# Kernel optimization log

Measured on AMD Instinct MI355X. Metric: run time of the kernel, lower is better.

The kernel has to match this reference:

```python
import jax, jax.numpy as jnp
import numpy as np

LSH_BUCKETS = 32
LSH_BANDWIDTH = 2.0
N_HASHES = 4
K_MAX = 64


def setup_inputs() -> dict:
    key0 = jax.random.key(0)
    kq, kk, kw = jax.random.split(key0, 3)
    B, L, D = 4, 4096, 64
    query = jax.random.normal(kq, (B, L, D), dtype=jnp.float32)
    key = jax.random.normal(kk, (B, L, D), dtype=jnp.float32)
    # learned LSH projection: maps binary features (D) -> N_HASHES hash values
    W = jax.random.normal(kw, (D, N_HASHES), dtype=jnp.float32)
    return {"query": query, "key": key, "W": W, "head_idx": 0}


def _lsh_hash(x_bin, W):
    # standard E2LSH-style hash: floor(<x, w> / bandwidth) mod n_buckets
    proj = x_bin @ W  # (B, L, N_HASHES)
    return jnp.floor(proj / LSH_BANDWIDTH).astype(jnp.int32) % LSH_BUCKETS


def reference(query, key, W, head_idx):
    B, L, _ = query.shape
    # binary_quantize: (x > 0).float()
    q_bin = (query > 0).astype(query.dtype)
    k_bin = (key > 0).astype(key.dtype)
    qh = _lsh_hash(q_bin, W)  # (B, L, N_HASHES) ints in [0, LSH_BUCKETS)
    kh = _lsh_hash(k_bin, W)
    # pack the N_HASHES hash values into one integer code per token;
    # codes equal  <=>  all hash values equal (values are in [0, LSH_BUCKETS))
    radix = (LSH_BUCKETS ** jnp.arange(N_HASHES)).astype(jnp.int32)  # (N_HASHES,)
    q_code = jnp.sum(qh * radix, axis=-1)  # (B, L)
    k_code = jnp.sum(kh * radix, axis=-1)  # (B, L)
    # match[b, i, j] = all hashes of query i equal hashes of key j
    match = q_code[:, :, None] == k_code[:, None, :]  # (B, L, L) bool
    # collect first K_MAX matching j per (b, i), pad with -1 (matches the
    # sequential early-break loop since j is scanned in increasing order)
    j_idx = jnp.arange(L, dtype=jnp.int32)
    score = jnp.where(match, j_idx[None, None, :], L)  # non-matches pushed to end
    first = jnp.sort(score, axis=-1)[:, :, :K_MAX]      # (B, L, K_MAX)
    candidates = jnp.where(first < L, first, -1)        # int32 indices, -1 pad
    return candidates
```

## Files before the change

### kernel.cpp

```cpp
#include <hip/hip_runtime.h>

#define KMAX 64
#define BB 4
#define LL 4096
#define DD 64
#define TOK (BB * LL)
#define QPW 4

typedef unsigned long long u64;

__global__ __launch_bounds__(256) void codes_kernel(
        const float* __restrict__ q,
        const float* __restrict__ k,
        const float* __restrict__ W,
        int* __restrict__ codes ) {
    __shared__ float sW[DD * 4];
    int tid = threadIdx.x;
    sW[tid] = W[tid];
    __syncthreads();

    int u = blockIdx.x * 256 + tid;
    const float* src = (u < TOK) ? q : k;
    int t = u & (TOK - 1);

    const float4* xp = (const float4*)(src + (size_t)t * DD);
    float4 x[16];
    #pragma unroll
    for (int i = 0; i < 16; ++i) x[i] = xp[i];

    float p0 = 0.f, p1 = 0.f, p2 = 0.f, p3 = 0.f;
    const float4* wrow = (const float4*)sW;
    #pragma unroll
    for (int d = 0; d < DD; ++d) {
        float xv = ((const float*)x)[d];
        float b = (xv > 0.f) ? 1.0f : 0.0f;
        float4 w = wrow[d];
        p0 = fmaf(b, w.x, p0);
        p1 = fmaf(b, w.y, p1);
        p2 = fmaf(b, w.z, p2);
        p3 = fmaf(b, w.w, p3);
    }
    int h0 = ((int)floorf(p0 * 0.5f)) & 31;
    int h1 = ((int)floorf(p1 * 0.5f)) & 31;
    int h2 = ((int)floorf(p2 * 0.5f)) & 31;
    int h3 = ((int)floorf(p3 * 0.5f)) & 31;
    codes[u] = h0 | (h1 << 5) | (h2 << 10) | (h3 << 15);
}

__global__ __launch_bounds__(256) void find_kernel(
        const int* __restrict__ qcodes,
        const int* __restrict__ kcodes,
        int* __restrict__ out) {
    int gtid = blockIdx.x * 256 + threadIdx.x;
    int wave = gtid >> 6;
    int lane = gtid & 63;
    int qbase = wave * QPW;
    int b = qbase >> 12;
    const int4* kc4 = (const int4*)(kcodes + b * LL);
    const int* qp = qcodes + qbase;
    int* outb = out + (size_t)qbase * KMAX;
    u64 lowmask = (1ull << lane) - 1ull;

    int4 kv[16];
    #pragma unroll
    for (int g = 0; g < 16; ++g) kv[g] = kc4[g * 64 + lane];

    int qc[QPW], cnt[QPW];
    #pragma unroll
    for (int i = 0; i < QPW; ++i) { qc[i] = qp[i]; cnt[i] = 0; }

    #pragma unroll
    for (int g = 0; g < 16; ++g) {
        bool a0 = (kv[g].x == qc[0]) | (kv[g].y == qc[0]) | (kv[g].z == qc[0]) | (kv[g].w == qc[0]);
        bool a1 = (kv[g].x == qc[1]) | (kv[g].y == qc[1]) | (kv[g].z == qc[1]) | (kv[g].w == qc[1]);
        bool a2 = (kv[g].x == qc[2]) | (kv[g].y == qc[2]) | (kv[g].z == qc[2]) | (kv[g].w == qc[2]);
        bool a3 = (kv[g].x == qc[3]) | (kv[g].y == qc[3]) | (kv[g].z == qc[3]) | (kv[g].w == qc[3]);
        if (__ballot(a0 | a1 | a2 | a3) == 0) continue;
        int j0 = g * 256 + lane * 4;
        #pragma unroll
        for (int i = 0; i < QPW; ++i) {
            if (cnt[i] >= KMAX) continue;
            bool m0 = (kv[g].x == qc[i]), m1 = (kv[g].y == qc[i]);
            bool m2 = (kv[g].z == qc[i]), m3 = (kv[g].w == qc[i]);
            if (__ballot(m0 | m1 | m2 | m3) == 0) continue;
            u64 b0 = __ballot(m0), b1 = __ballot(m1);
            u64 b2 = __ballot(m2), b3 = __ballot(m3);
            int before = __popcll(b0 & lowmask) + __popcll(b1 & lowmask)
                       + __popcll(b2 & lowmask) + __popcll(b3 & lowmask);
            int pos = cnt[i] + before;
            int* op = outb + i * KMAX;
            if (m0) { if (pos < KMAX) op[pos] = j0;     ++pos; }
            if (m1) { if (pos < KMAX) op[pos] = j0 + 1; ++pos; }
            if (m2) { if (pos < KMAX) op[pos] = j0 + 2; ++pos; }
            if (m3) { if (pos < KMAX) op[pos] = j0 + 3; ++pos; }
            cnt[i] += __popcll(b0) + __popcll(b1) + __popcll(b2) + __popcll(b3);
        }
    }
    #pragma unroll
    for (int i = 0; i < QPW; ++i) {
        int p = cnt[i] + lane;
        if (p < KMAX) outb[i * KMAX + p] = -1;
    }
}

extern "C" void kernel_launch(void* const* d_in, const int* in_sizes, int n_in,
                              void* d_out, int out_size, void* d_ws, size_t ws_size,
                              hipStream_t stream) {
    const float* q = (const float*)d_in[0];
    const float* k = (const float*)d_in[1];
    const float* W = (const float*)d_in[2];
    int* out = (int*)d_out;
    int* codes = (int*)d_ws;
    int* qcodes = codes;
    int* kcodes = codes + TOK;

    codes_kernel<<<(2 * TOK) / 256, 256, 0, stream>>>(q, k, W, codes);

    const int total_threads = (TOK / QPW) * 64;
    find_kernel<<<total_threads / 256, 256, 0, stream>>>(qcodes, kcodes, out);
}
```

Measured before the change: 20.90 us.

## Fuse query hash computation into the find kernel; hash only keys separately

Result: slower. 23.17 us (+10.9%).

```diff
diff --git a/kernel.cpp b/kernel.cpp
--- a/kernel.cpp
+++ b/kernel.cpp
@@ -9,21 +9,18 @@
 
 typedef unsigned long long u64;
 
-__global__ __launch_bounds__(256) void codes_kernel(
-        const float* __restrict__ q,
+__global__ __launch_bounds__(64) void kcodes_kernel(
         const float* __restrict__ k,
         const float* __restrict__ W,
-        int* __restrict__ codes ) {
+        int* __restrict__ kcodes ) {
     __shared__ float sW[DD * 4];
-    int tid = threadIdx.x;
-    sW[tid] = W[tid];
+    int lane = threadIdx.x;
+    #pragma unroll
+    for (int i = 0; i < 4; ++i) sW[i * 64 + lane] = W[i * 64 + lane];
     __syncthreads();
 
-    int u = blockIdx.x * 256 + tid;
-    const float* src = (u < TOK) ? q : k;
-    int t = u & (TOK - 1);
-
-    const float4* xp = (const float4*)(src + (size_t)t * DD);
+    int t = blockIdx.x * 64 + lane;
+    const float4* xp = (const float4*)(k + (size_t)t * DD);
     float4 x[16];
     #pragma unroll
     for (int i = 0; i < 16; ++i) x[i] = xp[i];
@@ -44,62 +41,96 @@
     int h1 = ((int)floorf(p1 * 0.5f)) & 31;
     int h2 = ((int)floorf(p2 * 0.5f)) & 31;
     int h3 = ((int)floorf(p3 * 0.5f)) & 31;
-    codes[u] = h0 | (h1 << 5) | (h2 << 10) | (h3 << 15);
+    kcodes[t] = h0 | (h1 << 5) | (h2 << 10) | (h3 << 15);
 }
 
 __global__ __launch_bounds__(256) void find_kernel(
-        const int* __restrict__ qcodes,
+        const float* __restrict__ q,
+        const float* __restrict__ W,
         const int* __restrict__ kcodes,
         int* __restrict__ out) {
-    int gtid = blockIdx.x * 256 + threadIdx.x;
+    __shared__ float sW[DD * 4];
+    int tid = threadIdx.x;
+    sW[tid] = W[tid];
+    __syncthreads();
+
+    int gtid = blockIdx.x * 256 + tid;
     int wave = gtid >> 6;
     int lane = gtid & 63;
     int qbase = wave * QPW;
     int b = qbase >> 12;
-    const int4* kc4 = (const int4*)(kcodes + b * LL);
-    const int* qp = qcodes + qbase;
-    int* outb = out + (size_t)qbase * KMAX;
-    u64 lowmask = (1ull << lane) - 1ull;
 
-    int4 kv[16];
-    #pragma unroll
-    for (int g = 0; g < 16; ++g) kv[g] = kc4[g * 64 + lane];
+    {
+        int myq = qbase + (lane >> 4);
+        const float4* xp = (const float4*)(q + (size_t)myq * DD);
+        float4 x[16];
+        #pragma unroll
+        for (int i = 0; i < 16; ++i) x[i] = xp[i];
+        float p0 = 0.f, p1 = 0.f, p2 = 0.f, p3 = 0.f;
+        const float4* wrow = (const float4*)sW;
+        #pragma unroll
+        for (int d = 0; d < DD; ++d) {
+            float xv = ((const float*)x)[d];
+            float bq = (xv > 0.f) ? 1.0f : 0.0f;
+            float4 w = wrow[d];
+            p0 = fmaf(bq, w.x, p0);
+            p1 = fmaf(bq, w.y, p1);
+            p2 = fmaf(bq, w.z, p2);
+            p3 = fmaf(bq, w.w, p3);
+        }
+        int h0 = ((int)floorf(p0 * 0.5f)) & 31;
+        int h1 = ((int)floorf(p1 * 0.5f)) & 31;
+        int h2 = ((int)floorf(p2 * 0.5f)) & 31;
+        int h3 = ((int)floorf(p3 * 0.5f)) & 31;
+        int mycode = h0 | (h1 << 5) | (h2 << 10) | (h3 << 15);
+        int c0 = __shfl(mycode, 0, 64);
+        int c1 = __shfl(mycode, 16, 64);
+        int c2 = __shfl(mycode, 32, 64);
+        int c3 = __shfl(mycode, 48, 64);
+        int qc_[QPW] = {c0, c1, c2, c3};
+        int cnt_[QPW] = {0, 0, 0, 0};
 
-    int qc[QPW], cnt[QPW];
-    #pragma unroll
-    for (int i = 0; i < QPW; ++i) { qc[i] = qp[i]; cnt[i] = 0; }
+        const int4* kc4 = (const int4*)(kcodes + b * LL);
+        int* outb = out + (size_t)qbase * KMAX;
+        u64 lowmask = (1ull << lane) - 1ull;
 
-    #pragma unroll
-    for (int g = 0; g < 16; ++g) {
-        bool a0 = (kv[g].x == qc[0]) | (kv[g].y == qc[0]) | (kv[g].z == qc[0]) | (kv[g].w == qc[0]);
-        bool a1 = (kv[g].x == qc[1]) | (kv[g].y == qc[1]) | (kv[g].z == qc[1]) | (kv[g].w == qc[1]);
-        bool a2 = (kv[g].x == qc[2]) | (kv[g].y == qc[2]) | (kv[g].z == qc[2]) | (kv[g].w == qc[2]);
-        bool a3 = (kv[g].x == qc[3]) | (kv[g].y == qc[3]) | (kv[g].z == qc[3]) | (kv[g].w == qc[3]);
-        if (__ballot(a0 | a1 | a2 | a3) == 0) continue;
-        int j0 = g * 256 + lane * 4;
+        int4 kv[16];
+        #pragma unroll
+        for (int g = 0; g < 16; ++g) kv[g] = kc4[g * 64 + lane];
+
+        #pragma unroll
+        for (int g = 0; g < 16; ++g) {
+            bool any = false;
+            #pragma unroll
+            for (int i = 0; i < QPW; ++i)
+                any |= (kv[g].x == qc_[i]) | (kv[g].y == qc_[i]) |
+                       (kv[g].z == qc_[i]) | (kv[g].w == qc_[i]);
+            if (__ballot(any) == 0) continue;
+            int j0 = g * 256 + lane * 4;
+            #pragma unroll
+            for (int i = 0; i < QPW; ++i) {
+                if (cnt_[i] >= KMAX) continue;
+                bool m0 = (kv[g].x == qc_[i]), m1 = (kv[g].y == qc_[i]);
+                bool m2 = (kv[g].z == qc_[i]), m3 = (kv[g].w == qc_[i]);
+                if (__ballot(m0 | m1 | m2 | m3) == 0) continue;
+                u64 b0 = __ballot(m0), b1 = __ballot(m1);
+                u64 b2 = __ballot(m2), b3 = __ballot(m3);
+                int before = __popcll(b0 & lowmask) + __popcll(b1 & lowmask)
+                           + __popcll(b2 & lowmask) + __popcll(b3 & lowmask);
+                int pos = cnt_[i] + before;
+                int* op = outb + i * KMAX;
+                if (m0) { if (pos < KMAX) op[pos] = j0;     ++pos; }
+                if (m1) { if (pos < KMAX) op[pos] = j0 + 1; ++pos; }
+                if (m2) { if (pos < KMAX) op[pos] = j0 + 2; ++pos; }
+                if (m3) { if (pos < KMAX) op[pos] = j0 + 3; ++pos; }
+                cnt_[i] += __popcll(b0) + __popcll(b1) + __popcll(b2) + __popcll(b3);
+            }
+        }
         #pragma unroll
         for (int i = 0; i < QPW; ++i) {
-            if (cnt[i] >= KMAX) continue;
-            bool m0 = (kv[g].x == qc[i]), m1 = (kv[g].y == qc[i]);
-            bool m2 = (kv[g].z == qc[i]), m3 = (kv[g].w == qc[i]);
-            if (__ballot(m0 | m1 | m2 | m3) == 0) continue;
-            u64 b0 = __ballot(m0), b1 = __ballot(m1);
-            u64 b2 = __ballot(m2), b3 = __ballot(m3);
-            int before = __popcll(b0 & lowmask) + __popcll(b1 & lowmask)
-                       + __popcll(b2 & lowmask) + __popcll(b3 & lowmask);
-            int pos = cnt[i] + before;
-            int* op = outb + i * KMAX;
-            if (m0) { if (pos < KMAX) op[pos] = j0;     ++pos; }
-            if (m1) { if (pos < KMAX) op[pos] = j0 + 1; ++pos; }
-            if (m2) { if (pos < KMAX) op[pos] = j0 + 2; ++pos; }
-            if (m3) { if (pos < KMAX) op[pos] = j0 + 3; ++pos; }
-            cnt[i] += __popcll(b0) + __popcll(b1) + __popcll(b2) + __popcll(b3);
+            int p = cnt_[i] + lane;
+            if (p < KMAX) outb[i * KMAX + p] = -1;
         }
-    }
-    #pragma unroll
-    for (int i = 0; i < QPW; ++i) {
-        int p = cnt[i] + lane;
-        if (p < KMAX) outb[i * KMAX + p] = -1;
     }
 }
 
@@ -110,12 +141,10 @@
     const float* k = (const float*)d_in[1];
     const float* W = (const float*)d_in[2];
     int* out = (int*)d_out;
-    int* codes = (int*)d_ws;
-    int* qcodes = codes;
-    int* kcodes = codes + TOK;
+    int* kcodes = (int*)d_ws;
 
-    codes_kernel<<<(2 * TOK) / 256, 256, 0, stream>>>(q, k, W, codes);
+    kcodes_kernel<<<TOK / 64, 64, 0, stream>>>(k, W, kcodes);
 
     const int total_threads = (TOK / QPW) * 64;
-    find_kernel<<<total_threads / 256, 256, 0, stream>>>(qcodes, kcodes, out);
+    find_kernel<<<total_threads / 256, 256, 0, stream>>>(q, W, kcodes, out);
 }
```
